# Optimization experiments

Measured on AMD Instinct MI355X. Metric: run time of the kernel, lower is better.

Reference implementation:

```python
import jax, jax.numpy as jnp
import numpy as np

L, D, H, V, B, S = 12, 768, 12, 50257, 1, 2048
F = 4 * D
HD = D // H
EPS = 1e-5
NEG = -1e38


def setup_inputs() -> dict:
    key = jax.random.key(0)
    ks = jax.random.split(key, 12)
    s = 0.02
    f32 = jnp.float32
    return {
        "x": jax.random.normal(ks[0], (B, S, D), f32),
        "ln1_g": jnp.ones((L, D), f32), "ln1_b": jnp.zeros((L, D), f32),
        "Wq": jax.random.normal(ks[1], (L, D, D), f32) * s,
        "Wk": jax.random.normal(ks[2], (L, D, D), f32) * s,
        "Wv": jax.random.normal(ks[3], (L, D, D), f32) * s,
        "Wo": jax.random.normal(ks[4], (L, D, D), f32) * s,
        "bo": jnp.zeros((L, D), f32),
        "ln2_g": jnp.ones((L, D), f32), "ln2_b": jnp.zeros((L, D), f32),
        "Wfc": jax.random.normal(ks[5], (L, D, F), f32) * s,
        "bfc": jnp.zeros((L, F), f32),
        "Wp": jax.random.normal(ks[6], (L, F, D), f32) * s,
        "bp": jnp.zeros((L, D), f32),
        "lnf_g": jnp.ones((D,), f32), "lnf_b": jnp.zeros((D,), f32),
        "Wlm": jax.random.normal(ks[7], (D, V), f32) * s,
    }


def _ln(h, g, b):
    mu = h.mean(-1, keepdims=True)
    var = ((h - mu) ** 2).mean(-1, keepdims=True)
    return (h - mu) * jax.lax.rsqrt(var + EPS) * g + b


def reference(x, ln1_g, ln1_b, Wq, Wk, Wv, Wo, bo, ln2_g, ln2_b,
              Wfc, bfc, Wp, bp, lnf_g, lnf_b, Wlm):
    Bx, Sx, Dx = x.shape
    # additive causal mask, NOTE: original has no 1/sqrt(head_dim) scaling
    mask = (1.0 - jnp.tril(jnp.ones((Sx, Sx), x.dtype))) * NEG

    def block(h, p):
        g1, b1, wq, wk, wv, wo, bo_, g2, b2, wfc, bfc_, wp, bp_ = p
        hn = _ln(h, g1, b1)
        def heads(w):  # [B,S,D] -> [B,H,S,hd]
            return (hn @ w).reshape(Bx, Sx, H, HD).transpose(0, 2, 1, 3)
        q, k, v = heads(wq), heads(wk), heads(wv)
        scores = jnp.einsum('bhqd,bhkd->bhqk', q, k) + mask
        probs = jax.nn.softmax(scores, axis=-1)
        attn = jnp.einsum('bhqk,bhkd->bhqd', probs, v)
        attn = attn.transpose(0, 2, 1, 3).reshape(Bx, Sx, Dx)
        h = h + attn @ wo + bo_
        hn2 = _ln(h, g2, b2)
        ff = jax.nn.gelu(hn2 @ wfc + bfc_, approximate=False) @ wp + bp_
        return h + ff, None

    h, _ = jax.lax.scan(
        block, x,
        (ln1_g, ln1_b, Wq, Wk, Wv, Wo, bo, ln2_g, ln2_b, Wfc, bfc, Wp, bp))
    return _ln(h, lnf_g, lnf_b) @ Wlm
```

## Files before the change

kernel.cpp:

```cpp
#include <hip/hip_runtime.h>
#include <hip/hip_bf16.h>
#include <math.h>

typedef unsigned short ushort;
typedef __attribute__((ext_vector_type(8))) short short8;
typedef __attribute__((ext_vector_type(4))) short short4v;
typedef __attribute__((ext_vector_type(4))) float f4v;

constexpr int SEQ = 2048;
constexpr int DM  = 768;
constexpr int NH  = 12;
constexpr int HDM = 64;
constexpr int FF  = 3072;
constexpr int NL  = 12;
constexpr int NV  = 50257;
constexpr int NVP = 50304;

__device__ inline ushort f2bf(float f) {
    union { float f; unsigned u; } v; v.f = f;
    unsigned r = v.u + 0x7fffu + ((v.u >> 16) & 1u);
    return (ushort)(r >> 16);
}

__device__ __forceinline__ void gld16(const ushort* g, ushort* l) {
    __builtin_amdgcn_global_load_lds(
        (const __attribute__((address_space(1))) void*)g,
        (__attribute__((address_space(3))) void*)l, 16, 0, 0);
}

__global__ __launch_bounds__(256) void ln_kernel(const float* __restrict__ x,
                                                 const float* __restrict__ g,
                                                 const float* __restrict__ b,
                                                 ushort* __restrict__ out) {
    int row = blockIdx.x;
    int t = threadIdx.x;
    const float* xr = x + (size_t)row * DM;
    float v0 = xr[t], v1 = xr[t + 256], v2 = xr[t + 512];
    float s = v0 + v1 + v2;
    float s2 = v0 * v0 + v1 * v1 + v2 * v2;
    for (int m = 1; m < 64; m <<= 1) { s += __shfl_xor(s, m); s2 += __shfl_xor(s2, m); }
    __shared__ float ls[4], ls2[4];
    int w = t >> 6;
    if ((t & 63) == 0) { ls[w] = s; ls2[w] = s2; }
    __syncthreads();
    s = ls[0] + ls[1] + ls[2] + ls[3];
    s2 = ls2[0] + ls2[1] + ls2[2] + ls2[3];
    float mu = s * (1.0f / DM);
    float var = s2 * (1.0f / DM) - mu * mu;
    float rs = rsqrtf(var + 1e-5f);
    ushort* o = out + (size_t)row * DM;
    o[t]       = f2bf((v0 - mu) * rs * g[t]       + b[t]);
    o[t + 256] = f2bf((v1 - mu) * rs * g[t + 256] + b[t + 256]);
    o[t + 512] = f2bf((v2 - mu) * rs * g[t + 512] + b[t + 512]);
}

struct CvtArgs {
    const float* src[7];
    ushort*      dst[7];
    long inL[7], outL[7];
    int  K[7], N[7], tk[7], tn[7];
    int  base[8];
};

__global__ __launch_bounds__(256) void cvt_all(CvtArgs a) {
    __shared__ ushort T[64][72];
    int idx = blockIdx.x;
    int seg = 0;
    #pragma unroll
    for (int i = 1; i < 7; ++i) if (idx >= a.base[i]) seg = i;
    int local = idx - a.base[seg];
    int K = a.K[seg], N = a.N[seg];
    int tk = a.tk[seg], tn = a.tn[seg];
    int k_t = local % tk;
    int rst = local / tk;
    int n_t = rst % tn;
    int l   = rst / tn;
    const float* ip = a.src[seg] + (size_t)l * a.inL[seg];
    ushort* op      = a.dst[seg] + (size_t)l * a.outL[seg];
    int kb = k_t * 64, nb = n_t * 64;
    int t = threadIdx.x;
    int nl = t & 63, ks = (t >> 6) * 16;
    int n = nb + nl;
    #pragma unroll
    for (int j = 0; j < 16; ++j) {
        float f = (n < N) ? ip[(size_t)(kb + ks + j) * N + n] : 0.f;
        T[nl][ks + j] = f2bf(f);
    }
    __syncthreads();
    int r = t >> 2, c4 = (t & 3) * 16;
    *(short8*)(op + (size_t)(nb + r) * K + kb + c4)     = *(const short8*)&T[r][c4];
    *(short8*)(op + (size_t)(nb + r) * K + kb + c4 + 8) = *(const short8*)&T[r][c4 + 8];
}

template <int BM, int BN, int EPI, bool DB, bool SWZ>
__global__ __launch_bounds__(256) void gemmT(const ushort* __restrict__ A,
                                             const ushort* __restrict__ Bt,
                                             const float* __restrict__ bias,
                                             const float* __restrict__ res,
                                             void* __restrict__ outp,
                                             ushort* __restrict__ vt,
                                             int M, int N, int K, int ldOut) {
    constexpr int FM = BM / 32;
    constexpr int FN = BN / 32;
    constexpr int NBUF = DB ? 2 : 1;
    constexpr int ASZ = BM * 64;
    constexpr int BSZ = BN * 64;
    __shared__ ushort As[NBUF * ASZ];
    __shared__ ushort Bs[NBUF * BSZ];
    int tid = threadIdx.x, lane = tid & 63, wave = tid >> 6;
    int wm = (wave >> 1) * (BM / 2), wn = (wave & 1) * (BN / 2);
    int mBase, nBase;
    if constexpr (SWZ) {
        int gx = gridDim.x;
        int nwg = gx * gridDim.y;
        int flat = blockIdx.y * gx + blockIdx.x;
        int xcd = flat & 7, idx = flat >> 3;
        int q = nwg >> 3, r = nwg & 7;
        int wg = (xcd < r ? xcd * (q + 1) : r * (q + 1) + (xcd - r) * q) + idx;
        mBase = (wg % gx) * BM;
        nBase = (wg / gx) * BN;
    } else {
        mBase = blockIdx.x * BM;
        nBase = blockIdx.y * BN;
    }
    int lr = lane & 15, lg = lane >> 4;
    int swz = (lr & 7) << 3;

    f4v acc[FM][FN];
    #pragma unroll
    for (int i = 0; i < FM; ++i)
        #pragma unroll
        for (int j = 0; j < FN; ++j) acc[i][j] = (f4v){0.f, 0.f, 0.f, 0.f};

    int cBase = wave * 64 + lane;

    auto stage = [&](int kb, int buf) {
        #pragma unroll
        for (int i = 0; i < BM / 32; ++i) {
            int c = i * 256 + cBase;
            int row = c >> 3;
            int kc = (c & 7) ^ (row & 7);
            gld16(A + (size_t)(mBase + row) * K + kb + kc * 8,
                  As + buf * ASZ + (size_t)(i * 256 + wave * 64) * 8);
        }
        #pragma unroll
        for (int i = 0; i < BN / 32; ++i) {
            int c = i * 256 + cBase;
            int row = c >> 3;
            int kc = (c & 7) ^ (row & 7);
            gld16(Bt + (size_t)(nBase + row) * K + kb + kc * 8,
                  Bs + buf * BSZ + (size_t)(i * 256 + wave * 64) * 8);
        }
    };
    auto compute = [&](int buf) {
        #pragma unroll
        for (int kk = 0; kk < 2; ++kk) {
            short8 a[FM], b[FN];
            #pragma unroll
            for (int fr = 0; fr < FM; ++fr)
                a[fr] = *(const short8*)(As + buf * ASZ + (wm + fr * 16 + lr) * 64 + ((((kk * 4 + lg) << 3)) ^ swz));
            #pragma unroll
            for (int fc = 0; fc < FN; ++fc)
                b[fc] = *(const short8*)(Bs + buf * BSZ + (wn + fc * 16 + lr) * 64 + ((((kk * 4 + lg) << 3)) ^ swz));
            #pragma unroll
            for (int fr = 0; fr < FM; ++fr)
                #pragma unroll
                for (int fc = 0; fc < FN; ++fc)
                    acc[fr][fc] = __builtin_amdgcn_mfma_f32_16x16x32_bf16(a[fr], b[fc], acc[fr][fc], 0, 0, 0);
        }
    };

    if constexpr (DB) {
        stage(0, 0);
        __syncthreads();
        int cur = 0;
        for (int kb = 0; kb < K; kb += 64) {
            if (kb + 64 < K) stage(kb + 64, cur ^ 1);
            compute(cur);
            __syncthreads();
            cur ^= 1;
        }
    } else {
        for (int kb = 0; kb < K; kb += 64) {
            stage(kb, 0);
            __syncthreads();
            compute(0);
            __syncthreads();
        }
    }

    if constexpr (EPI == 4) {
        if (nBase < 1536) {
            #pragma unroll
            for (int fr = 0; fr < FM; ++fr)
                #pragma unroll
                for (int fc = 0; fc < FN; ++fc)
                    #pragma unroll
                    for (int r = 0; r < 4; ++r) {
                        int row = mBase + wm + fr * 16 + 4 * lg + r;
                        int col = nBase + wn + fc * 16 + lr;
                        ((ushort*)outp)[(size_t)row * ldOut + col] = f2bf(acc[fr][fc][r]);
                    }
        } else {
            #pragma unroll
            for (int fr = 0; fr < FM; ++fr)
                #pragma unroll
                for (int fc = 0; fc < FN; ++fc) {
                    short4v pk;
                    #pragma unroll
                    for (int r = 0; r < 4; ++r) pk[r] = (short)f2bf(acc[fr][fc][r]);
                    int d  = nBase - 1536 + wn + fc * 16 + lr;
                    int m0 = mBase + wm + fr * 16 + 4 * lg;
                    *(short4v*)(vt + (size_t)d * SEQ + m0) = pk;
                }
        }
        return;
    }

    #pragma unroll
    for (int fr = 0; fr < FM; ++fr)
        #pragma unroll
        for (int fc = 0; fc < FN; ++fc)
            #pragma unroll
            for (int r = 0; r < 4; ++r) {
                int row = mBase + wm + fr * 16 + 4 * lg + r;
                int col = nBase + wn + fc * 16 + lr;
                float v = acc[fr][fc][r];
                if constexpr (EPI == 0) {
                    ((ushort*)outp)[(size_t)row * ldOut + col] = f2bf(v);
                } else if constexpr (EPI == 1) {
                    v += bias[col] + res[(size_t)row * ldOut + col];
                    ((float*)outp)[(size_t)row * ldOut + col] = v;
                } else if constexpr (EPI == 2) {
                    v += bias[col];
                    v = 0.5f * v * (1.f + erff(v * 0.70710678118f));
                    ((ushort*)outp)[(size_t)row * ldOut + col] = f2bf(v);
                } else {
                    if (col < N) ((float*)outp)[(size_t)row * ldOut + col] = v;
                }
            }
}

__global__ __launch_bounds__(256) void attn_v6(const ushort* __restrict__ Qg,
                                               const ushort* __restrict__ Kg,
                                               const ushort* __restrict__ Vt,
                                               ushort* __restrict__ Og) {
    __shared__ ushort Ks[2 * 4096];
    __shared__ ushort Vs[2 * 4096];
    __shared__ ushort Ps[4 * 16 * 64];
    int tid = threadIdx.x, lane = tid & 63, wave = tid >> 6;
    int flat = blockIdx.x;
    int qb   = (SEQ / 64) - 1 - (flat / NH);
    int head = flat % NH;
    int lr = lane & 15, lg = lane >> 4;
    int qr0 = qb * 64 + wave * 16;
    int hoff = head * HDM;
    int swz = (lr & 7) << 3;

    short8 qf0 = *(const short8*)(Qg + (size_t)(qr0 + lr) * 2304 + hoff + lg * 8);
    short8 qf1 = *(const short8*)(Qg + (size_t)(qr0 + lr) * 2304 + hoff + 32 + lg * 8);

    const f4v fz = {0.f, 0.f, 0.f, 0.f};
    f4v o[4];
    o[0] = fz; o[1] = fz; o[2] = fz; o[3] = fz;
    float mrow[4] = {-1e30f, -1e30f, -1e30f, -1e30f};
    float lsum[4] = {0.f, 0.f, 0.f, 0.f};

    int c0 = wave * 64 + lane;
    int c1 = c0 + 256;
    int r0 = c0 >> 3, kc0 = ((c0 & 7) ^ (r0 & 7)) * 8;
    int r1 = c1 >> 3, kc1 = ((c1 & 7) ^ (r1 & 7)) * 8;

    auto stageKV = [&](int kb, int buf) {
        gld16(Kg + (size_t)(kb * 64 + r0) * 2304 + hoff + kc0, Ks + buf * 4096 + wave * 512);
        gld16(Kg + (size_t)(kb * 64 + r1) * 2304 + hoff + kc1, Ks + buf * 4096 + 2048 + wave * 512);
        gld16(Vt + (size_t)(hoff + r0) * SEQ + kb * 64 + kc0,  Vs + buf * 4096 + wave * 512);
        gld16(Vt + (size_t)(hoff + r1) * SEQ + kb * 64 + kc1,  Vs + buf * 4096 + 2048 + wave * 512);
    };

    stageKV(0, 0);
    __syncthreads();
    int cur = 0;

    for (int kb = 0; kb <= qb; ++kb) {
        if (kb < qb) stageKV(kb + 1, cur ^ 1);

        f4v s[4];
        #pragma unroll
        for (int n = 0; n < 4; ++n) {
            const ushort* kr = Ks + cur * 4096 + (n * 16 + lr) * 64;
            short8 k0 = *(const short8*)(kr + ((lg << 3) ^ swz));
            short8 k1 = *(const short8*)(kr + ((((4 + lg) << 3)) ^ swz));
            f4v z = fz;
            z = __builtin_amdgcn_mfma_f32_16x16x32_bf16(qf0, k0, z, 0, 0, 0);
            s[n] = __builtin_amdgcn_mfma_f32_16x16x32_bf16(qf1, k1, z, 0, 0, 0);
        }
        if (kb == qb) {
            #pragma unroll
            for (int n = 0; n < 4; ++n)
                #pragma unroll
                for (int r = 0; r < 4; ++r) {
                    int col = kb * 64 + n * 16 + lr;
                    int row = qr0 + 4 * lg + r;
                    if (col > row) s[n][r] = -1e38f;
                }
        }

        int sub = lr & 7, hi = lr >> 3;
        #pragma unroll
        for (int r = 0; r < 4; ++r) {
            float mx = fmaxf(fmaxf(s[0][r], s[1][r]), fmaxf(s[2][r], s[3][r]));
            mx = fmaxf(mx, __shfl_xor(mx, 1));
            mx = fmaxf(mx, __shfl_xor(mx, 2));
            mx = fmaxf(mx, __shfl_xor(mx, 4));
            mx = fmaxf(mx, __shfl_xor(mx, 8));
            float mnew = fmaxf(mrow[r], mx);
            float corr = __expf(mrow[r] - mnew);
            float ps0 = __expf(s[0][r] - mnew);
            float ps1 = __expf(s[1][r] - mnew);
            float ps2 = __expf(s[2][r] - mnew);
            float ps3 = __expf(s[3][r] - mnew);
            float rs = ps0 + ps1 + ps2 + ps3;
            rs += __shfl_xor(rs, 1);
            rs += __shfl_xor(rs, 2);
            rs += __shfl_xor(rs, 4);
            rs += __shfl_xor(rs, 8);
            lsum[r] = lsum[r] * corr + rs;
            mrow[r] = mnew;
            o[0][r] *= corr; o[1][r] *= corr; o[2][r] *= corr; o[3][r] *= corr;
            int prow = 4 * lg + r;
            ushort* pb = Ps + wave * 1024 + prow * 64;
            int px = prow & 7;
            pb[(((0 + hi) ^ px) << 3) | sub] = f2bf(ps0);
            pb[(((2 + hi) ^ px) << 3) | sub] = f2bf(ps1);
            pb[(((4 + hi) ^ px) << 3) | sub] = f2bf(ps2);
            pb[(((6 + hi) ^ px) << 3) | sub] = f2bf(ps3);
        }
        __syncthreads();

        #pragma unroll
        for (int kk = 0; kk < 2; ++kk) {
            short8 pa = *(const short8*)(Ps + wave * 1024 + lr * 64 + ((((kk * 4 + lg) << 3)) ^ swz));
            #pragma unroll
            for (int dn = 0; dn < 4; ++dn) {
                short8 vb = *(const short8*)(Vs + cur * 4096 + (dn * 16 + lr) * 64 + ((((kk * 4 + lg) << 3)) ^ swz));
                o[dn] = __builtin_amdgcn_mfma_f32_16x16x32_bf16(pa, vb, o[dn], 0, 0, 0);
            }
        }
        __syncthreads();
        cur ^= 1;
    }

    #pragma unroll
    for (int dn = 0; dn < 4; ++dn)
        #pragma unroll
        for (int r = 0; r < 4; ++r) {
            int row = qr0 + 4 * lg + r;
            Og[(size_t)row * DM + hoff + dn * 16 + lr] = f2bf(o[dn][r] / lsum[r]);
        }
}

template <int EPI>
__global__ __launch_bounds__(256) void gemm64(const ushort* __restrict__ A,
                                              const float* __restrict__ B,
                                              const float* __restrict__ bias,
                                              const float* __restrict__ res,
                                              void* __restrict__ outp,
                                              int M, int N, int K) {
    __shared__ ushort As[64][64];
    __shared__ ushort Bs[64][72];
    int tid = threadIdx.x;
    int lane = tid & 63, wave = tid >> 6;
    int wm = (wave >> 1) * 32, wn = (wave & 1) * 32;
    int mBase = blockIdx.x * 64, nBase = blockIdx.y * 64;
    int lr = lane & 15, lg = lane >> 4;

    const f4v fz = {0.f, 0.f, 0.f, 0.f};
    f4v acc[2][2];
    acc[0][0] = fz; acc[0][1] = fz; acc[1][0] = fz; acc[1][1] = fz;

    int ar = tid >> 2, ac = (tid & 3) * 16;
    int br = tid >> 2, bc = (tid & 3) * 16;

    for (int kb = 0; kb < K; kb += 64) {
        const short8* ag = (const short8*)(A + (size_t)(mBase + ar) * K + kb + ac);
        *(short8*)&As[ar][ac]     = ag[0];
        *(short8*)&As[ar][ac + 8] = ag[1];
        if constexpr (EPI == 3) {
            #pragma unroll
            for (int j = 0; j < 16; ++j) {
                int col = nBase + bc + j;
                float f = (col < N) ? B[(size_t)(kb + br) * N + col] : 0.f;
                Bs[bc + j][br] = f2bf(f);
            }
        } else {
            const float4* bg = (const float4*)(B + (size_t)(kb + br) * N + nBase + bc);
            float fv[16];
            *(float4*)&fv[0]  = bg[0];
            *(float4*)&fv[4]  = bg[1];
            *(float4*)&fv[8]  = bg[2];
            *(float4*)&fv[12] = bg[3];
            #pragma unroll
            for (int j = 0; j < 16; ++j) Bs[bc + j][br] = f2bf(fv[j]);
        }
        __syncthreads();
        #pragma unroll
        for (int kk = 0; kk < 2; ++kk) {
            short8 a0 = *(const short8*)&As[wm + lr][kk * 32 + lg * 8];
            short8 a1 = *(const short8*)&As[wm + 16 + lr][kk * 32 + lg * 8];
            short8 b0 = *(const short8*)&Bs[wn + lr][kk * 32 + lg * 8];
            short8 b1 = *(const short8*)&Bs[wn + 16 + lr][kk * 32 + lg * 8];
            acc[0][0] = __builtin_amdgcn_mfma_f32_16x16x32_bf16(a0, b0, acc[0][0], 0, 0, 0);
            acc[0][1] = __builtin_amdgcn_mfma_f32_16x16x32_bf16(a0, b1, acc[0][1], 0, 0, 0);
            acc[1][0] = __builtin_amdgcn_mfma_f32_16x16x32_bf16(a1, b0, acc[1][0], 0, 0, 0);
            acc[1][1] = __builtin_amdgcn_mfma_f32_16x16x32_bf16(a1, b1, acc[1][1], 0, 0, 0);
        }
        __syncthreads();
    }

    #pragma unroll
    for (int fm = 0; fm < 2; ++fm)
        #pragma unroll
        for (int fn = 0; fn < 2; ++fn)
            #pragma unroll
            for (int r = 0; r < 4; ++r) {
                int row = mBase + wm + fm * 16 + 4 * lg + r;
                int col = nBase + wn + fn * 16 + lr;
                float v = acc[fm][fn][r];
                if constexpr (EPI == 0) {
                    ((ushort*)outp)[(size_t)row * N + col] = f2bf(v);
                } else if constexpr (EPI == 1) {
                    v += bias[col] + res[(size_t)row * N + col];
                    ((float*)outp)[(size_t)row * N + col] = v;
                } else if constexpr (EPI == 2) {
                    v += bias[col];
                    v = 0.5f * v * (1.f + erff(v * 0.70710678118f));
                    ((ushort*)outp)[(size_t)row * N + col] = f2bf(v);
                } else {
                    if (col < N) ((float*)outp)[(size_t)row * N + col] = v;
                }
            }
}

__global__ __launch_bounds__(256) void attn_stage(const ushort* __restrict__ Qg,
                                                  const ushort* __restrict__ Kg,
                                                  const ushort* __restrict__ Vg,
                                                  ushort* __restrict__ Og,
                                                  int ld) {
    __shared__ ushort Ks[64][64];
    __shared__ ushort Vs[64][72];
    __shared__ ushort Ps[4][16][64];
    int tid = threadIdx.x, lane = tid & 63, wave = tid >> 6;
    int qb = blockIdx.x, head = blockIdx.y;
    int lr = lane & 15, lg = lane >> 4;
    int qr0 = qb * 64 + wave * 16;
    size_t hoff = (size_t)head * HDM;

    short8 qf0 = *(const short8*)(Qg + (size_t)(qr0 + lr) * ld + hoff + lg * 8);
    short8 qf1 = *(const short8*)(Qg + (size_t)(qr0 + lr) * ld + hoff + 32 + lg * 8);

    const f4v fz = {0.f, 0.f, 0.f, 0.f};
    f4v o[4];
    o[0] = fz; o[1] = fz; o[2] = fz; o[3] = fz;
    float mrow[4] = {-1e30f, -1e30f, -1e30f, -1e30f};
    float lsum[4] = {0.f, 0.f, 0.f, 0.f};

    int r_ = tid >> 2, c_ = (tid & 3) * 16;

    for (int kb = 0; kb <= qb; ++kb) {
        const short8* kg = (const short8*)(Kg + (size_t)(kb * 64 + r_) * ld + hoff + c_);
        *(short8*)&Ks[r_][c_]     = kg[0];
        *(short8*)&Ks[r_][c_ + 8] = kg[1];
        const short8* vg = (const short8*)(Vg + (size_t)(kb * 64 + r_) * ld + hoff + c_);
        short8 v0 = vg[0], v1 = vg[1];
        #pragma unroll
        for (int j = 0; j < 8; ++j) {
            Vs[c_ + j][r_]     = (ushort)v0[j];
            Vs[c_ + 8 + j][r_] = (ushort)v1[j];
        }
        __syncthreads();

        f4v s[4];
        #pragma unroll
        for (int n = 0; n < 4; ++n) {
            short8 k0 = *(const short8*)&Ks[n * 16 + lr][lg * 8];
            short8 k1 = *(const short8*)&Ks[n * 16 + lr][32 + lg * 8];
            f4v z = fz;
            z = __builtin_amdgcn_mfma_f32_16x16x32_bf16(qf0, k0, z, 0, 0, 0);
            s[n] = __builtin_amdgcn_mfma_f32_16x16x32_bf16(qf1, k1, z, 0, 0, 0);
        }
        if (kb == qb) {
            #pragma unroll
            for (int n = 0; n < 4; ++n)
                #pragma unroll
                for (int r = 0; r < 4; ++r) {
                    int col = kb * 64 + n * 16 + lr;
                    int row = qr0 + 4 * lg + r;
                    if (col > row) s[n][r] = -1e38f;
                }
        }

        #pragma unroll
        for (int r = 0; r < 4; ++r) {
            float mx = fmaxf(fmaxf(s[0][r], s[1][r]), fmaxf(s[2][r], s[3][r]));
            mx = fmaxf(mx, __shfl_xor(mx, 1));
            mx = fmaxf(mx, __shfl_xor(mx, 2));
            mx = fmaxf(mx, __shfl_xor(mx, 4));
            mx = fmaxf(mx, __shfl_xor(mx, 8));
            float mnew = fmaxf(mrow[r], mx);
            float corr = __expf(mrow[r] - mnew);
            float ps0 = __expf(s[0][r] - mnew);
            float ps1 = __expf(s[1][r] - mnew);
            float ps2 = __expf(s[2][r] - mnew);
            float ps3 = __expf(s[3][r] - mnew);
            float rs = ps0 + ps1 + ps2 + ps3;
            rs += __shfl_xor(rs, 1);
            rs += __shfl_xor(rs, 2);
            rs += __shfl_xor(rs, 4);
            rs += __shfl_xor(rs, 8);
            lsum[r] = lsum[r] * corr + rs;
            mrow[r] = mnew;
            o[0][r] *= corr; o[1][r] *= corr; o[2][r] *= corr; o[3][r] *= corr;
            Ps[wave][4 * lg + r][0 * 16 + lr] = f2bf(ps0);
            Ps[wave][4 * lg + r][1 * 16 + lr] = f2bf(ps1);
            Ps[wave][4 * lg + r][2 * 16 + lr] = f2bf(ps2);
            Ps[wave][4 * lg + r][3 * 16 + lr] = f2bf(ps3);
        }
        __syncthreads();

        #pragma unroll
        for (int kk = 0; kk < 2; ++kk) {
            short8 pa = *(const short8*)&Ps[wave][lr][kk * 32 + lg * 8];
            #pragma unroll
            for (int dn = 0; dn < 4; ++dn) {
                short8 vb = *(const short8*)&Vs[dn * 16 + lr][kk * 32 + lg * 8];
                o[dn] = __builtin_amdgcn_mfma_f32_16x16x32_bf16(pa, vb, o[dn], 0, 0, 0);
            }
        }
        __syncthreads();
    }

    #pragma unroll
    for (int dn = 0; dn < 4; ++dn)
        #pragma unroll
        for (int r = 0; r < 4; ++r) {
            int row = qr0 + 4 * lg + r;
            Og[(size_t)row * DM + hoff + dn * 16 + lr] = f2bf(o[dn][r] / lsum[r]);
        }
}

extern "C" void kernel_launch(void* const* d_in, const int* in_sizes, int n_in,
                              void* d_out, int out_size, void* d_ws, size_t ws_size,
                              hipStream_t stream) {
    const float* x     = (const float*)d_in[0];
    const float* ln1_g = (const float*)d_in[1];
    const float* ln1_b = (const float*)d_in[2];
    const float* Wq    = (const float*)d_in[3];
    const float* Wk    = (const float*)d_in[4];
    const float* Wv    = (const float*)d_in[5];
    const float* Wo    = (const float*)d_in[6];
    const float* bo    = (const float*)d_in[7];
    const float* ln2_g = (const float*)d_in[8];
    const float* ln2_b = (const float*)d_in[9];
    const float* Wfc   = (const float*)d_in[10];
    const float* bfc   = (const float*)d_in[11];
    const float* Wp    = (const float*)d_in[12];
    const float* bp    = (const float*)d_in[13];
    const float* lnf_g = (const float*)d_in[14];
    const float* lnf_b = (const float*)d_in[15];
    const float* Wlm   = (const float*)d_in[16];

    dim3 blk(256);

    size_t offs[12];
    size_t need = 0;
    size_t sizes[11] = {
        (size_t)SEQ * DM * 4,
        (size_t)SEQ * DM * 2,
        (size_t)SEQ * 2304 * 2,
        (size_t)SEQ * DM * 2,
        (size_t)SEQ * FF * 2,
        (size_t)DM * SEQ * 2,
        (size_t)NL * 2304 * DM * 2,
        (size_t)NL * DM * DM * 2,
        (size_t)NL * FF * DM * 2,
        (size_t)NL * DM * FF * 2,
        (size_t)NVP * DM * 2,
    };
    for (int i = 0; i < 11; ++i) { offs[i] = need; need += sizes[i]; }
    offs[11] = need;

    if (ws_size >= need) {
        char* ws = (char*)d_ws;
        float*  h    = (float*)(ws + offs[0]);
        ushort* hn   = (ushort*)(ws + offs[1]);
        ushort* qkv  = (ushort*)(ws + offs[2]);
        ushort* ab_  = (ushort*)(ws + offs[3]);
        ushort* fb_  = (ushort*)(ws + offs[4]);
        ushort* vt   = (ushort*)(ws + offs[5]);
        ushort* qkvw = (ushort*)(ws + offs[6]);
        ushort* wow  = (ushort*)(ws + offs[7]);
        ushort* fcw  = (ushort*)(ws + offs[8]);
        ushort* wpw  = (ushort*)(ws + offs[9]);
        ushort* lmw  = (ushort*)(ws + offs[10]);

        hipMemcpyAsync(h, x, (size_t)SEQ * DM * 4, hipMemcpyDeviceToDevice, stream);

        CvtArgs ca;
        const float* srcs[7] = {Wq, Wk, Wv, Wo, Wfc, Wp, Wlm};
        ushort* dsts[7] = {qkvw, qkvw + DM * DM, qkvw + 2 * DM * DM, wow, fcw, wpw, lmw};
        long inLs[7]  = {(long)DM * DM, (long)DM * DM, (long)DM * DM, (long)DM * DM,
                         (long)DM * FF, (long)FF * DM, 0};
        long outLs[7] = {(long)2304 * DM, (long)2304 * DM, (long)2304 * DM, (long)DM * DM,
                         (long)FF * DM, (long)DM * FF, 0};
        int Ks_[7] = {DM, DM, DM, DM, DM, FF, DM};
        int Ns_[7] = {DM, DM, DM, DM, FF, DM, NV};
        int tks[7] = {12, 12, 12, 12, 12, 48, 12};
        int tns[7] = {12, 12, 12, 12, 48, 12, 786};
        int lays[7] = {NL, NL, NL, NL, NL, NL, 1};
        int total = 0;
        for (int i = 0; i < 7; ++i) {
            ca.src[i] = srcs[i]; ca.dst[i] = dsts[i];
            ca.inL[i] = inLs[i]; ca.outL[i] = outLs[i];
            ca.K[i] = Ks_[i]; ca.N[i] = Ns_[i]; ca.tk[i] = tks[i]; ca.tn[i] = tns[i];
            ca.base[i] = total;
            total += tks[i] * tns[i] * lays[i];
        }
        ca.base[7] = total;
        cvt_all<<<dim3(total), blk, 0, stream>>>(ca);

        for (int l = 0; l < NL; ++l) {
            const ushort* qw = qkvw + (size_t)l * 2304 * DM;
            ln_kernel<<<SEQ, blk, 0, stream>>>(h, ln1_g + l * DM, ln1_b + l * DM, hn);
            gemmT<64, 64, 4, true, false><<<dim3(32, 36), blk, 0, stream>>>(hn, qw, nullptr, nullptr, qkv, vt, SEQ, 2304, DM, 2304);
            attn_v6<<<dim3((SEQ / 64) * NH), blk, 0, stream>>>(qkv, qkv + 768, vt, ab_);
            gemmT<64, 64, 1, true, false><<<dim3(32, 12), blk, 0, stream>>>(ab_, wow + (size_t)l * DM * DM, bo + l * DM, h, h, nullptr, SEQ, DM, DM, DM);
            ln_kernel<<<SEQ, blk, 0, stream>>>(h, ln2_g + l * DM, ln2_b + l * DM, hn);
            gemmT<64, 64, 2, true, false><<<dim3(32, 48), blk, 0, stream>>>(hn, fcw + (size_t)l * FF * DM, bfc + l * FF, nullptr, fb_, nullptr, SEQ, FF, DM, FF);
            gemmT<64, 64, 1, true, false><<<dim3(32, 12), blk, 0, stream>>>(fb_, wpw + (size_t)l * DM * FF, bp + l * DM, h, h, nullptr, SEQ, DM, FF, DM);
        }
        ln_kernel<<<SEQ, blk, 0, stream>>>(h, lnf_g, lnf_b, hn);
        gemmT<128, 128, 3, true, true><<<dim3(16, NVP / 128), blk, 0, stream>>>(hn, lmw, nullptr, nullptr, d_out, nullptr, SEQ, NV, DM, NV);
        return;
    }

    char* ws = (char*)d_ws;
    float*  h   = (float*)ws;   ws += (size_t)SEQ * DM * 4;
    ushort* hn  = (ushort*)ws;  ws += (size_t)SEQ * DM * 2;
    ushort* qb_ = (ushort*)ws;  ws += (size_t)SEQ * DM * 2;
    ushort* kb_ = (ushort*)ws;  ws += (size_t)SEQ * DM * 2;
    ushort* vb_ = (ushort*)ws;  ws += (size_t)SEQ * DM * 2;
    ushort* ab_ = (ushort*)ws;  ws += (size_t)SEQ * DM * 2;
    ushort* fb_ = (ushort*)ws;  ws += (size_t)SEQ * FF * 2;

    hipMemcpyAsync(h, x, (size_t)SEQ * DM * 4, hipMemcpyDeviceToDevice, stream);

    dim3 gdd(SEQ / 64, DM / 64);
    dim3 gdf(SEQ / 64, FF / 64);
    dim3 gda(SEQ / 64, NH);
    dim3 gdl(SEQ / 64, (NV + 63) / 64);

    for (int l = 0; l < NL; ++l) {
        ln_kernel<<<SEQ, blk, 0, stream>>>(h, ln1_g + l * DM, ln1_b + l * DM, hn);
        gemm64<0><<<gdd, blk, 0, stream>>>(hn, Wq + (size_t)l * DM * DM, nullptr, nullptr, qb_, SEQ, DM, DM);
        gemm64<0><<<gdd, blk, 0, stream>>>(hn, Wk + (size_t)l * DM * DM, nullptr, nullptr, kb_, SEQ, DM, DM);
        gemm64<0><<<gdd, blk, 0, stream>>>(hn, Wv + (size_t)l * DM * DM, nullptr, nullptr, vb_, SEQ, DM, DM);
        attn_stage<<<gda, blk, 0, stream>>>(qb_, kb_, vb_, ab_, DM);
        gemm64<1><<<gdd, blk, 0, stream>>>(ab_, Wo + (size_t)l * DM * DM, bo + l * DM, h, h, SEQ, DM, DM);
        ln_kernel<<<SEQ, blk, 0, stream>>>(h, ln2_g + l * DM, ln2_b + l * DM, hn);
        gemm64<2><<<gdf, blk, 0, stream>>>(hn, Wfc + (size_t)l * DM * FF, bfc + l * FF, nullptr, fb_, SEQ, FF, DM);
        gemm64<1><<<gdd, blk, 0, stream>>>(fb_, Wp + (size_t)l * FF * DM, bp + l * DM, h, h, SEQ, DM, FF);
    }
    ln_kernel<<<SEQ, blk, 0, stream>>>(h, lnf_g, lnf_b, hn);
    gemm64<3><<<gdl, blk, 0, stream>>>(hn, Wlm, nullptr, nullptr, d_out, SEQ, NV, DM);
}
```

Before: 2.605 ms.

## Halve attention query tile to 32 rows, widen LM-head tile, add occupancy hint

Attention now runs 32-query tiles with two waves per block, doubling the grid so the causal workload is split more finely across CUs. The LM-head GEMM switches to a 128x256 tile without double buffering, and the vocab padding grows to a multiple of 256 to fit it. gemmT gains a min-blocks-per-CU launch bound of 2, which can force register limits or spills. In the attention kernel, smaller query tiles make each K/V tile staged into LDS serve fewer queries, so reuse drops, and the last-tile masking now also covers query tiles that do not align to 64.

```diff
diff --git a/kernel.cpp b/kernel.cpp
--- a/kernel.cpp
+++ b/kernel.cpp
@@ -14,7 +14,7 @@
 constexpr int FF  = 3072;
 constexpr int NL  = 12;
 constexpr int NV  = 50257;
-constexpr int NVP = 50304;
+constexpr int NVP = 50432;
 
 __device__ inline ushort f2bf(float f) {
     union { float f; unsigned u; } v; v.f = f;
@@ -93,13 +93,13 @@
 }
 
 template <int BM, int BN, int EPI, bool DB, bool SWZ>
-__global__ __launch_bounds__(256) void gemmT(const ushort* __restrict__ A,
-                                             const ushort* __restrict__ Bt,
-                                             const float* __restrict__ bias,
-                                             const float* __restrict__ res,
-                                             void* __restrict__ outp,
-                                             ushort* __restrict__ vt,
-                                             int M, int N, int K, int ldOut) {
+__global__ __launch_bounds__(256, 2) void gemmT(const ushort* __restrict__ A,
+                                                const ushort* __restrict__ Bt,
+                                                const float* __restrict__ bias,
+                                                const float* __restrict__ res,
+                                                void* __restrict__ outp,
+                                                ushort* __restrict__ vt,
+                                                int M, int N, int K, int ldOut) {
     constexpr int FM = BM / 32;
     constexpr int FN = BN / 32;
     constexpr int NBUF = DB ? 2 : 1;
@@ -241,21 +241,22 @@
             }
 }
 
-__global__ __launch_bounds__(256) void attn_v6(const ushort* __restrict__ Qg,
+__global__ __launch_bounds__(128) void attn_v7(const ushort* __restrict__ Qg,
                                                const ushort* __restrict__ Kg,
                                                const ushort* __restrict__ Vt,
                                                ushort* __restrict__ Og) {
     __shared__ ushort Ks[2 * 4096];
     __shared__ ushort Vs[2 * 4096];
-    __shared__ ushort Ps[4 * 16 * 64];
+    __shared__ ushort Ps[2 * 1024];
     int tid = threadIdx.x, lane = tid & 63, wave = tid >> 6;
     int flat = blockIdx.x;
-    int qb   = (SEQ / 64) - 1 - (flat / NH);
+    int qt   = (SEQ / 32) - 1 - (flat / NH);
     int head = flat % NH;
     int lr = lane & 15, lg = lane >> 4;
-    int qr0 = qb * 64 + wave * 16;
+    int qr0 = qt * 32 + wave * 16;
     int hoff = head * HDM;
     int swz = (lr & 7) << 3;
+    int ktiles = (qt * 32 + 31) / 64 + 1;
 
     short8 qf0 = *(const short8*)(Qg + (size_t)(qr0 + lr) * 2304 + hoff + lg * 8);
     short8 qf1 = *(const short8*)(Qg + (size_t)(qr0 + lr) * 2304 + hoff + 32 + lg * 8);
@@ -266,24 +267,25 @@
     float mrow[4] = {-1e30f, -1e30f, -1e30f, -1e30f};
     float lsum[4] = {0.f, 0.f, 0.f, 0.f};
 
-    int c0 = wave * 64 + lane;
-    int c1 = c0 + 256;
-    int r0 = c0 >> 3, kc0 = ((c0 & 7) ^ (r0 & 7)) * 8;
-    int r1 = c1 >> 3, kc1 = ((c1 & 7) ^ (r1 & 7)) * 8;
-
     auto stageKV = [&](int kb, int buf) {
-        gld16(Kg + (size_t)(kb * 64 + r0) * 2304 + hoff + kc0, Ks + buf * 4096 + wave * 512);
-        gld16(Kg + (size_t)(kb * 64 + r1) * 2304 + hoff + kc1, Ks + buf * 4096 + 2048 + wave * 512);
-        gld16(Vt + (size_t)(hoff + r0) * SEQ + kb * 64 + kc0,  Vs + buf * 4096 + wave * 512);
-        gld16(Vt + (size_t)(hoff + r1) * SEQ + kb * 64 + kc1,  Vs + buf * 4096 + 2048 + wave * 512);
+        #pragma unroll
+        for (int j = 0; j < 4; ++j) {
+            int cc = j * 128 + wave * 64 + lane;
+            int row = cc >> 3;
+            int kc = (cc & 7) ^ (row & 7);
+            gld16(Kg + (size_t)(kb * 64 + row) * 2304 + hoff + kc * 8,
+                  Ks + buf * 4096 + (size_t)(j * 128 + wave * 64) * 8);
+            gld16(Vt + (size_t)(hoff + row) * SEQ + kb * 64 + kc * 8,
+                  Vs + buf * 4096 + (size_t)(j * 128 + wave * 64) * 8);
+        }
     };
 
     stageKV(0, 0);
     __syncthreads();
     int cur = 0;
 
-    for (int kb = 0; kb <= qb; ++kb) {
-        if (kb < qb) stageKV(kb + 1, cur ^ 1);
+    for (int kb = 0; kb < ktiles; ++kb) {
+        if (kb + 1 < ktiles) stageKV(kb + 1, cur ^ 1);
 
         f4v s[4];
         #pragma unroll
@@ -295,7 +297,7 @@
             z = __builtin_amdgcn_mfma_f32_16x16x32_bf16(qf0, k0, z, 0, 0, 0);
             s[n] = __builtin_amdgcn_mfma_f32_16x16x32_bf16(qf1, k1, z, 0, 0, 0);
         }
-        if (kb == qb) {
+        if (kb == ktiles - 1) {
             #pragma unroll
             for (int n = 0; n < 4; ++n)
                 #pragma unroll
@@ -616,7 +618,7 @@
         int Ks_[7] = {DM, DM, DM, DM, DM, FF, DM};
         int Ns_[7] = {DM, DM, DM, DM, FF, DM, NV};
         int tks[7] = {12, 12, 12, 12, 12, 48, 12};
-        int tns[7] = {12, 12, 12, 12, 48, 12, 786};
+        int tns[7] = {12, 12, 12, 12, 48, 12, NVP / 64};
         int lays[7] = {NL, NL, NL, NL, NL, NL, 1};
         int total = 0;
         for (int i = 0; i < 7; ++i) {
@@ -633,14 +635,14 @@
             const ushort* qw = qkvw + (size_t)l * 2304 * DM;
             ln_kernel<<<SEQ, blk, 0, stream>>>(h, ln1_g + l * DM, ln1_b + l * DM, hn);
             gemmT<64, 64, 4, true, false><<<dim3(32, 36), blk, 0, stream>>>(hn, qw, nullptr, nullptr, qkv, vt, SEQ, 2304, DM, 2304);
-            attn_v6<<<dim3((SEQ / 64) * NH), blk, 0, stream>>>(qkv, qkv + 768, vt, ab_);
+            attn_v7<<<dim3((SEQ / 32) * NH), dim3(128), 0, stream>>>(qkv, qkv + 768, vt, ab_);
             gemmT<64, 64, 1, true, false><<<dim3(32, 12), blk, 0, stream>>>(ab_, wow + (size_t)l * DM * DM, bo + l * DM, h, h, nullptr, SEQ, DM, DM, DM);
             ln_kernel<<<SEQ, blk, 0, stream>>>(h, ln2_g + l * DM, ln2_b + l * DM, hn);
             gemmT<64, 64, 2, true, false><<<dim3(32, 48), blk, 0, stream>>>(hn, fcw + (size_t)l * FF * DM, bfc + l * FF, nullptr, fb_, nullptr, SEQ, FF, DM, FF);
             gemmT<64, 64, 1, true, false><<<dim3(32, 12), blk, 0, stream>>>(fb_, wpw + (size_t)l * DM * FF, bp + l * DM, h, h, nullptr, SEQ, DM, FF, DM);
         }
         ln_kernel<<<SEQ, blk, 0, stream>>>(h, lnf_g, lnf_b, hn);
-        gemmT<128, 128, 3, true, true><<<dim3(16, NVP / 128), blk, 0, stream>>>(hn, lmw, nullptr, nullptr, d_out, nullptr, SEQ, NV, DM, NV);
+        gemmT<128, 256, 3, false, true><<<dim3(16, NVP / 256), blk, 0, stream>>>(hn, lmw, nullptr, nullptr, d_out, nullptr, SEQ, NV, DM, NV);
         return;
     }
 
```

Measured after the change: 2.518 ms. 3.3% less time.
